# Kernel tuning notes

Measured on AMD Instinct MI355X. Metric: run time of the kernel, lower is better.

The kernel has to match this reference:

```python
import jax, jax.numpy as jnp
import numpy as np

EMBED = 768
HEADS = 12
HEAD_DIM = EMBED // HEADS

def setup_inputs() -> dict:
    key = jax.random.key(0)
    k1, k2, k3, k4 = jax.random.split(key, 4)
    x = jax.random.normal(k1, (8, 1024, EMBED), dtype=jnp.float32)
    # qkv Linear (no bias per qkv_bias=False); proj Linear with bias
    w_qkv = jax.random.normal(k2, (EMBED, 3 * EMBED), dtype=jnp.float32) * 0.02
    w_proj = jax.random.normal(k3, (EMBED, EMBED), dtype=jnp.float32) * 0.02
    b_proj = jax.random.normal(k4, (EMBED,), dtype=jnp.float32) * 0.02
    return {"x": x, "w_qkv": w_qkv, "w_proj": w_proj, "b_proj": b_proj}

def reference(x, w_qkv, w_proj, b_proj):
    b, n, e = x.shape
    h, d = HEADS, HEAD_DIM
    scale = d ** (-0.5)
    qkv = x @ w_qkv                                    # [b, n, 3*e]
    qkv = qkv.reshape(b, n, 3, h, d)                   # (qkv h d) split order
    q, k, v = (jnp.transpose(qkv[:, :, i], (0, 2, 1, 3)) for i in range(3))  # [b,h,n,d]
    dots = jnp.einsum('bhid,bhjd->bhij', q, k) * scale
    attn = jax.nn.softmax(dots, axis=-1)               # dropout p=0 -> identity
    out = jnp.einsum('bhij,bhjd->bhid', attn, v)       # [b,h,n,d]
    out = jnp.transpose(out, (0, 2, 1, 3)).reshape(b, n, e)
    return out @ w_proj + b_proj
```

## Files before the change

### kernel.cpp

```cpp
#include <hip/hip_runtime.h>

typedef _Float16 f16;
typedef _Float16 half8 __attribute__((ext_vector_type(8)));
typedef _Float16 half4v __attribute__((ext_vector_type(4)));
typedef float f32x4 __attribute__((ext_vector_type(4)));

#define MFMA16(a,b,c) __builtin_amdgcn_mfma_f32_16x16x32_f16((a),(b),(c),0,0,0)

__device__ __forceinline__ void gload_lds16(const f16* g, f16* l) {
    __builtin_amdgcn_global_load_lds(
        (const __attribute__((address_space(1))) unsigned int*)g,
        (__attribute__((address_space(3))) unsigned int*)l, 16, 0, 0);
}

__global__ void cast_f32_to_f16(const float* __restrict__ in, f16* __restrict__ out, int n4) {
    int i = blockIdx.x * blockDim.x + threadIdx.x;
    if (i < n4) {
        float4 v = ((const float4*)in)[i];
        half4v h;
        h.x = (f16)v.x; h.y = (f16)v.y; h.z = (f16)v.z; h.w = (f16)v.w;
        ((half4v*)out)[i] = h;
    }
}

__global__ void transpose_cast(const float* __restrict__ in, f16* __restrict__ out, int K, int N) {
    __shared__ f16 tile[32][33];
    int n0 = blockIdx.x * 32, k0 = blockIdx.y * 32;
    int tx = threadIdx.x & 31, ty = threadIdx.x >> 5;
    for (int r = ty; r < 32; r += 8)
        tile[r][tx] = (f16)in[(size_t)(k0 + r) * N + (n0 + tx)];
    __syncthreads();
    for (int r = ty; r < 32; r += 8)
        out[(size_t)(n0 + r) * K + (k0 + tx)] = tile[tx][r];
}

template<int MODE>
__global__ __launch_bounds__(256, 3)
void gemm_bt(const f16* __restrict__ A, const f16* __restrict__ Bt,
             f16* __restrict__ qbuf, f16* __restrict__ kbuf, f16* __restrict__ vtbuf,
             float* __restrict__ out, const float* __restrict__ bias)
{
    constexpr int K = 768;
    constexpr int NX = (MODE == 0) ? 18 : 6;
    constexpr int NWG = NX * 64;
    __shared__ __align__(16) char smem[49152];
    f16* As = (f16*)smem;
    f16* Bs = (f16*)(smem + 24576);
    const int tid  = threadIdx.x;
    const int lane = tid & 63, wave = tid >> 6;
    const int wm = wave >> 1, wn = wave & 1;
    const int l15 = lane & 15, l4 = lane >> 4;

    const int bid = blockIdx.x;
    const int swz = (bid & 7) * (NWG / 8) + (bid >> 3);
    const int m0 = (swz / NX) * 128, n0 = (swz % NX) * 128;

    const int srow  = lane >> 2;
    const int sslot = lane & 3;

    f32x4 acc[4][4] = {};

    #define GSTAGE(buf, kt) do {                                                     \
        _Pragma("unroll")                                                            \
        for (int i = 0; i < 2; ++i) {                                                \
            int rbase = i * 64 + wave * 16;                                          \
            int row = rbase + srow;                                                  \
            gload_lds16(A  + (size_t)(m0 + row) * K + (kt) + sslot * 8, &As[(buf) * 4096 + rbase * 32]); \
            gload_lds16(Bt + (size_t)(n0 + row) * K + (kt) + sslot * 8, &Bs[(buf) * 4096 + rbase * 32]); \
        }                                                                            \
    } while (0)

    GSTAGE(0, 0);
    GSTAGE(1, 32);

    int cur = 0;
    for (int t = 0; t < 24; ++t) {
        if (t < 23) asm volatile("s_waitcnt vmcnt(4)" ::: "memory");
        else        asm volatile("s_waitcnt vmcnt(0)" ::: "memory");
        __builtin_amdgcn_s_barrier();
        if (t < 22) {
            int nb = cur + 2; if (nb >= 3) nb -= 3;
            GSTAGE(nb, (t + 2) * 32);
        }
        half8 af[4], bf[4];
        #pragma unroll
        for (int mi = 0; mi < 4; mi++) af[mi] = *(const half8*)&As[cur*4096 + (wm*64 + mi*16 + l15) * 32 + l4*8];
        #pragma unroll
        for (int ni = 0; ni < 4; ni++) bf[ni] = *(const half8*)&Bs[cur*4096 + (wn*64 + ni*16 + l15) * 32 + l4*8];
        #pragma unroll
        for (int mi = 0; mi < 4; mi++)
            #pragma unroll
            for (int ni = 0; ni < 4; ni++)
                acc[mi][ni] = MFMA16(af[mi], bf[ni], acc[mi][ni]);
        if (++cur >= 3) cur = 0;
    }
    #undef GSTAGE

    if (MODE == 0) {
        __syncthreads();
        f16* sC = (f16*)smem;
        const int t3 = n0 / 768;
        const int bb = m0 >> 10;
        const int mo = m0 & 1023;
        const int h0 = (n0 - t3 * 768) >> 6;

        if (t3 < 2) {
            #pragma unroll
            for (int mi = 0; mi < 4; mi++)
                #pragma unroll
                for (int ni = 0; ni < 4; ni++)
                    #pragma unroll
                    for (int r = 0; r < 4; r++) {
                        int row = wm*64 + mi*16 + l4*4 + r;
                        int col = wn*64 + ni*16 + l15;
                        sC[row * 136 + col] = (f16)acc[mi][ni][r];
                    }
            __syncthreads();
            f16* outb = (t3 == 0) ? qbuf : kbuf;
            #pragma unroll
            for (int hc = 0; hc < 2; hc++) {
                f16* base = outb + ((size_t)(bb * 12 + h0 + hc) * 1024 + mo) * 64;
                #pragma unroll
                for (int i = 0; i < 4; i++) {
                    int row = wave * 32 + i * 8 + (lane >> 3);
                    int cc  = (lane & 7) * 8;
                    half8 v = *(const half8*)&sC[row * 136 + hc * 64 + cc];
                    *(half8*)(base + row * 64 + cc) = v;
                }
            }
        } else {
            #pragma unroll
            for (int mi = 0; mi < 4; mi++)
                #pragma unroll
                for (int ni = 0; ni < 4; ni++) {
                    int row0 = wm*64 + mi*16 + l4*4;
                    int col  = wn*64 + ni*16 + l15;
                    half4v pk;
                    #pragma unroll
                    for (int r = 0; r < 4; r++) pk[r] = (f16)acc[mi][ni][r];
                    *(half4v*)&sC[col * 136 + row0] = pk;
                }
            __syncthreads();
            #pragma unroll
            for (int i = 0; i < 8; i++) {
                int col = wave * 32 + i * 4 + (lane >> 4);
                int rc  = (lane & 15) * 8;
                half8 v = *(const half8*)&sC[col * 136 + rc];
                int head = h0 + (col >> 6), dd = col & 63;
                *(half8*)(vtbuf + ((size_t)(bb * 12 + head) * 64 + dd) * 1024 + mo + rc) = v;
            }
        }
    } else {
        #pragma unroll
        for (int mi = 0; mi < 4; mi++)
            #pragma unroll
            for (int ni = 0; ni < 4; ni++)
                #pragma unroll
                for (int r = 0; r < 4; r++) {
                    int gm = m0 + wm*64 + mi*16 + l4*4 + r;
                    int gn = n0 + wn*64 + ni*16 + l15;
                    out[(size_t)gm * 768 + gn] = acc[mi][ni][r] + bias[gn];
                }
    }
}

__global__ __launch_bounds__(256, 4)
void attn_kernel(const f16* __restrict__ qbuf, const f16* __restrict__ kbuf,
                 const f16* __restrict__ vtbuf, f16* __restrict__ obuf)
{
    __shared__ __align__(16) f16 Ks[2][4096];
    __shared__ __align__(16) f16 Vs[2][4096];
    __shared__ __align__(16) char sPall[4 * 2048];
    const int tid = threadIdx.x;
    const int lane = tid & 63, wave = tid >> 6;
    char* sP = sPall + wave * 2048;
    const int bh = blockIdx.y;
    const int b = bh / 12, h = bh % 12;
    const int q0 = blockIdx.x * 64 + wave * 16;
    const int l15 = lane & 15, l4 = lane >> 4;

    const f16* Q  = qbuf  + (size_t)bh * 65536;
    const f16* Kp = kbuf  + (size_t)bh * 65536;
    const f16* Vt = vtbuf + (size_t)bh * 65536;

    const f16 slh = (f16)(0.125f * 1.44269504089f);
    half8 aq[2];
    aq[0] = *(const half8*)&Q[(q0 + l15) * 64 + l4 * 8];
    aq[1] = *(const half8*)&Q[(q0 + l15) * 64 + 32 + l4 * 8];
    #pragma unroll
    for (int j = 0; j < 8; j++) { aq[0][j] *= slh; aq[1][j] *= slh; }

    const int srow8 = lane >> 3;
    const int c16   = (lane & 7) ^ srow8;

    f32x4 o[4] = {};
    float mrq = -1e30f, lrq = 0.f;

    #define STAGE(buf, kv) do {                                                     \
        _Pragma("unroll")                                                           \
        for (int i = 0; i < 2; ++i) {                                               \
            int rbase = wave * 16 + i * 8;                                          \
            int rl = rbase + srow8;                                                 \
            gload_lds16(Kp + (size_t)((kv) + rl) * 64 + c16 * 8, &Ks[buf][rbase * 64]); \
            gload_lds16(Vt + (size_t)rl * 1024 + (kv) + c16 * 8, &Vs[buf][rbase * 64]); \
        }                                                                           \
    } while (0)

    STAGE(0, 0);
    __syncthreads();

    for (int t = 0; t < 16; ++t) {
        const int cur = t & 1;
        if (t < 15) STAGE(cur ^ 1, (t + 1) * 64);

        const char* Kb = (const char*)&Ks[cur][0];
        const char* Vb = (const char*)&Vs[cur][0];

        f32x4 st[4];
        #pragma unroll
        for (int ni = 0; ni < 4; ni++) {
            int row = ni * 16 + l15;
            int sw = ((row & 7) << 4);
            half8 k0 = *(const half8*)(Kb + row * 128 + ((l4 * 16) ^ sw));
            half8 k1 = *(const half8*)(Kb + row * 128 + ((64 + l4 * 16) ^ sw));
            f32x4 z = {0.f, 0.f, 0.f, 0.f};
            z = MFMA16(k0, aq[0], z);
            st[ni] = MFMA16(k1, aq[1], z);
        }

        float m16 = st[0][0];
        #pragma unroll
        for (int ni = 0; ni < 4; ni++)
            #pragma unroll
            for (int r = 0; r < 4; r++) m16 = fmaxf(m16, st[ni][r]);
        m16 = fmaxf(m16, __shfl_xor(m16, 16));
        m16 = fmaxf(m16, __shfl_xor(m16, 32));

        if (!__all(m16 - mrq <= 11.0f)) {
            float mnew = fmaxf(mrq, m16);
            float alpha = exp2f(mrq - mnew);
            mrq = mnew;
            lrq *= alpha;
            float alr[4];
            #pragma unroll
            for (int r = 0; r < 4; r++) alr[r] = __shfl(alpha, l4*4 + r);
            #pragma unroll
            for (int nd = 0; nd < 4; nd++)
                #pragma unroll
                for (int r = 0; r < 4; r++) o[nd][r] *= alr[r];
        }

        float rs = 0.f;
        #pragma unroll
        for (int ni = 0; ni < 4; ni++)
            #pragma unroll
            for (int r = 0; r < 4; r++) {
                float p = exp2f(st[ni][r] - mrq);
                st[ni][r] = p;
                rs += p;
            }
        rs += __shfl_xor(rs, 16);
        rs += __shfl_xor(rs, 32);
        lrq += rs;

        #pragma unroll
        for (int ni = 0; ni < 4; ni++) {
            half4v pk;
            #pragma unroll
            for (int r = 0; r < 4; r++) pk[r] = (f16)st[ni][r];
            int byte = (l15 * 128 + (ni*16 + l4*4) * 2) ^ ((l15 & 7) << 4);
            *(half4v*)(sP + byte) = pk;
        }

        #pragma unroll
        for (int kk = 0; kk < 2; kk++) {
            int pbyte = (l15 * 128 + (kk*32 + l4*8) * 2) ^ ((l15 & 7) << 4);
            half8 pa = *(const half8*)(sP + pbyte);
            #pragma unroll
            for (int nd = 0; nd < 4; nd++) {
                int row = nd * 16 + l15;
                half8 bv = *(const half8*)(Vb + row * 128 + ((kk*64 + l4*16) ^ ((row & 7) << 4)));
                o[nd] = MFMA16(pa, bv, o[nd]);
            }
        }

        __syncthreads();
    }
    #undef STAGE

    float lrr[4];
    #pragma unroll
    for (int r = 0; r < 4; r++) lrr[r] = 1.f / __shfl(lrq, l4*4 + r);

    f16* Op = obuf + (size_t)b * 1024 * 768 + h * 64;
    #pragma unroll
    for (int nd = 0; nd < 4; nd++)
        #pragma unroll
        for (int r = 0; r < 4; r++) {
            int qi = q0 + l4 * 4 + r;
            int d  = nd * 16 + l15;
            Op[(size_t)qi * 768 + d] = (f16)(o[nd][r] * lrr[r]);
        }
}

extern "C" void kernel_launch(void* const* d_in, const int* in_sizes, int n_in,
                              void* d_out, int out_size, void* d_ws, size_t ws_size,
                              hipStream_t stream) {
    const float* x      = (const float*)d_in[0];
    const float* w_qkv  = (const float*)d_in[1];
    const float* w_proj = (const float*)d_in[2];
    const float* b_proj = (const float*)d_in[3];
    float* out = (float*)d_out;
    char* ws = (char*)d_ws;

    f16* x_h      = (f16*)(ws + 0);
    f16* w_qkv_t  = (f16*)(ws + 12582912);
    f16* w_proj_t = (f16*)(ws + 16121856);
    f16* qb       = (f16*)(ws + 17301504);
    f16* kb       = (f16*)(ws + 29884416);
    f16* vtb      = (f16*)(ws + 42467328);
    f16* ob       = (f16*)(ws + 55050240);

    cast_f32_to_f16<<<dim3(6144), dim3(256), 0, stream>>>(x, x_h, 6291456 / 4);
    transpose_cast<<<dim3(2304 / 32, 768 / 32), dim3(256), 0, stream>>>(w_qkv, w_qkv_t, 768, 2304);
    transpose_cast<<<dim3(768 / 32, 768 / 32), dim3(256), 0, stream>>>(w_proj, w_proj_t, 768, 768);
    gemm_bt<0><<<dim3(18 * 64), dim3(256), 0, stream>>>(
        x_h, w_qkv_t, qb, kb, vtb, nullptr, nullptr);
    attn_kernel<<<dim3(1024 / 64, 96), dim3(256), 0, stream>>>(qb, kb, vtb, ob);
    gemm_bt<1><<<dim3(6 * 64), dim3(256), 0, stream>>>(
        ob, w_proj_t, nullptr, nullptr, nullptr, out, b_proj);
}
```

Before: 137.7 us.

## Fold max subtraction into MFMA init and compute row sums via MFMA

The running max is now folded into the QK^T MFMA accumulator init, so scores arrive already shifted and no per-element subtraction is needed. The softmax row sum is computed by an extra MFMA of the fp16 P tile against a ones vector instead of scalar adds plus cross-lane shuffles. Exponentials are packed with cvt_pkrtz. The row sum now comes from the rounded fp16 probabilities and uses round-toward-zero conversion, which slightly changes numerics. The initial max of 0 relies on the lazy-rescale threshold.

Result: no change. 135.8 us (-1.4%).

```diff
diff --git a/kernel.cpp b/kernel.cpp
--- a/kernel.cpp
+++ b/kernel.cpp
@@ -3,6 +3,7 @@
 typedef _Float16 f16;
 typedef _Float16 half8 __attribute__((ext_vector_type(8)));
 typedef _Float16 half4v __attribute__((ext_vector_type(4)));
+typedef __fp16 fp16x2 __attribute__((ext_vector_type(2)));
 typedef float f32x4 __attribute__((ext_vector_type(4)));
 
 #define MFMA16(a,b,c) __builtin_amdgcn_mfma_f32_16x16x32_f16((a),(b),(c),0,0,0)
@@ -190,11 +191,16 @@
     #pragma unroll
     for (int j = 0; j < 8; j++) { aq[0][j] *= slh; aq[1][j] *= slh; }
 
+    half8 ones;
+    #pragma unroll
+    for (int j = 0; j < 8; j++) ones[j] = (f16)1.0f;
+
     const int srow8 = lane >> 3;
     const int c16   = (lane & 7) ^ srow8;
 
     f32x4 o[4] = {};
-    float mrq = -1e30f, lrq = 0.f;
+    float lr4[4] = {0.f, 0.f, 0.f, 0.f};
+    float mrq = 0.f;
 
     #define STAGE(buf, kv) do {                                                     \
         _Pragma("unroll")                                                           \
@@ -217,61 +223,57 @@
         const char* Vb = (const char*)&Vs[cur][0];
 
         f32x4 st[4];
+        f32x4 zinit = {-mrq, -mrq, -mrq, -mrq};
         #pragma unroll
         for (int ni = 0; ni < 4; ni++) {
             int row = ni * 16 + l15;
             int sw = ((row & 7) << 4);
             half8 k0 = *(const half8*)(Kb + row * 128 + ((l4 * 16) ^ sw));
             half8 k1 = *(const half8*)(Kb + row * 128 + ((64 + l4 * 16) ^ sw));
-            f32x4 z = {0.f, 0.f, 0.f, 0.f};
-            z = MFMA16(k0, aq[0], z);
+            f32x4 z = MFMA16(k0, aq[0], zinit);
             st[ni] = MFMA16(k1, aq[1], z);
         }
 
-        float m16 = st[0][0];
-        #pragma unroll
-        for (int ni = 0; ni < 4; ni++)
-            #pragma unroll
-            for (int r = 0; r < 4; r++) m16 = fmaxf(m16, st[ni][r]);
+        float m16 = fmaxf(fmaxf(st[0][0], st[0][1]), fmaxf(st[0][2], st[0][3]));
+        #pragma unroll
+        for (int ni = 1; ni < 4; ni++) {
+            float a = fmaxf(fmaxf(st[ni][0], st[ni][1]), fmaxf(st[ni][2], st[ni][3]));
+            m16 = fmaxf(m16, a);
+        }
         m16 = fmaxf(m16, __shfl_xor(m16, 16));
         m16 = fmaxf(m16, __shfl_xor(m16, 32));
 
-        if (!__all(m16 - mrq <= 11.0f)) {
-            float mnew = fmaxf(mrq, m16);
-            float alpha = exp2f(mrq - mnew);
-            mrq = mnew;
-            lrq *= alpha;
+        if (!__all(m16 <= 11.0f)) {
+            float d = fmaxf(m16, 0.f);
+            float alpha = exp2f(-d);
+            mrq += d;
+            #pragma unroll
+            for (int ni = 0; ni < 4; ni++)
+                #pragma unroll
+                for (int r = 0; r < 4; r++) st[ni][r] -= d;
             float alr[4];
             #pragma unroll
             for (int r = 0; r < 4; r++) alr[r] = __shfl(alpha, l4*4 + r);
             #pragma unroll
+            for (int r = 0; r < 4; r++) lr4[r] *= alr[r];
+            #pragma unroll
             for (int nd = 0; nd < 4; nd++)
                 #pragma unroll
                 for (int r = 0; r < 4; r++) o[nd][r] *= alr[r];
         }
 
-        float rs = 0.f;
-        #pragma unroll
-        for (int ni = 0; ni < 4; ni++)
-            #pragma unroll
-            for (int r = 0; r < 4; r++) {
-                float p = exp2f(st[ni][r] - mrq);
-                st[ni][r] = p;
-                rs += p;
-            }
-        rs += __shfl_xor(rs, 16);
-        rs += __shfl_xor(rs, 32);
-        lrq += rs;
-
         #pragma unroll
         for (int ni = 0; ni < 4; ni++) {
-            half4v pk;
-            #pragma unroll
-            for (int r = 0; r < 4; r++) pk[r] = (f16)st[ni][r];
+            fp16x2 lo = __builtin_amdgcn_cvt_pkrtz(exp2f(st[ni][0]), exp2f(st[ni][1]));
+            fp16x2 hi = __builtin_amdgcn_cvt_pkrtz(exp2f(st[ni][2]), exp2f(st[ni][3]));
+            uint2 u;
+            u.x = __builtin_bit_cast(unsigned int, lo);
+            u.y = __builtin_bit_cast(unsigned int, hi);
             int byte = (l15 * 128 + (ni*16 + l4*4) * 2) ^ ((l15 & 7) << 4);
-            *(half4v*)(sP + byte) = pk;
-        }
-
+            *(uint2*)(sP + byte) = u;
+        }
+
+        f32x4 racc = {0.f, 0.f, 0.f, 0.f};
         #pragma unroll
         for (int kk = 0; kk < 2; kk++) {
             int pbyte = (l15 * 128 + (kk*32 + l4*8) * 2) ^ ((l15 & 7) << 4);
@@ -282,7 +284,10 @@
                 half8 bv = *(const half8*)(Vb + row * 128 + ((kk*64 + l4*16) ^ ((row & 7) << 4)));
                 o[nd] = MFMA16(pa, bv, o[nd]);
             }
-        }
+            racc = MFMA16(pa, ones, racc);
+        }
+        #pragma unroll
+        for (int r = 0; r < 4; r++) lr4[r] += racc[r];
 
         __syncthreads();
     }
@@ -290,7 +295,7 @@
 
     float lrr[4];
     #pragma unroll
-    for (int r = 0; r < 4; r++) lrr[r] = 1.f / __shfl(lrq, l4*4 + r);
+    for (int r = 0; r < 4; r++) lrr[r] = 1.f / lr4[r];
 
     f16* Op = obuf + (size_t)b * 1024 * 768 + h * 64;
     #pragma unroll
```

## Switch attention kernel to 32x32 MFMA tiles with 128-query blocks

Applied to the files above, without the earlier changes.

Rewrites the attention kernel around the 32x32x16 MFMA so each wave handles 32 query rows and each block 128 queries. Each K/V tile staged in LDS is therefore reused by twice as many queries, and fewer instructions are spent on the score and PV products. The running max is folded into the accumulator initial value, exponentials are packed with cvt_pkrtz, and the grid is reordered so blocks for the same head launch together. In exchange the kernel uses more registers and LDS, the launch bound drops from 4 to 3 blocks, and the grid shrinks to 768 blocks, which may reduce occupancy.

After: 127.6 us. 1.08x faster.

```diff
diff --git a/kernel.cpp b/kernel.cpp
--- a/kernel.cpp
+++ b/kernel.cpp
@@ -3,9 +3,12 @@
 typedef _Float16 f16;
 typedef _Float16 half8 __attribute__((ext_vector_type(8)));
 typedef _Float16 half4v __attribute__((ext_vector_type(4)));
+typedef __fp16 fp16x2 __attribute__((ext_vector_type(2)));
 typedef float f32x4 __attribute__((ext_vector_type(4)));
+typedef float f32x16 __attribute__((ext_vector_type(16)));
 
 #define MFMA16(a,b,c) __builtin_amdgcn_mfma_f32_16x16x32_f16((a),(b),(c),0,0,0)
+#define MFMA32(a,b,c) __builtin_amdgcn_mfma_f32_32x32x16_f16((a),(b),(c),0,0,0)
 
 __device__ __forceinline__ void gload_lds16(const f16* g, f16* l) {
     __builtin_amdgcn_global_load_lds(
@@ -164,37 +167,40 @@
     }
 }
 
-__global__ __launch_bounds__(256, 4)
+__global__ __launch_bounds__(256, 3)
 void attn_kernel(const f16* __restrict__ qbuf, const f16* __restrict__ kbuf,
                  const f16* __restrict__ vtbuf, f16* __restrict__ obuf)
 {
     __shared__ __align__(16) f16 Ks[2][4096];
     __shared__ __align__(16) f16 Vs[2][4096];
-    __shared__ __align__(16) char sPall[4 * 2048];
+    __shared__ __align__(16) char sPall[4 * 4096];
     const int tid = threadIdx.x;
     const int lane = tid & 63, wave = tid >> 6;
-    char* sP = sPall + wave * 2048;
-    const int bh = blockIdx.y;
+    char* sP = sPall + wave * 4096;
+    const int bh = blockIdx.x;
     const int b = bh / 12, h = bh % 12;
-    const int q0 = blockIdx.x * 64 + wave * 16;
-    const int l15 = lane & 15, l4 = lane >> 4;
+    const int q0 = blockIdx.y * 128 + wave * 32;
+    const int l31 = lane & 31, hi = lane >> 5;
+    const int sw0 = (l31 & 7) << 4;
 
     const f16* Q  = qbuf  + (size_t)bh * 65536;
     const f16* Kp = kbuf  + (size_t)bh * 65536;
     const f16* Vt = vtbuf + (size_t)bh * 65536;
 
     const f16 slh = (f16)(0.125f * 1.44269504089f);
-    half8 aq[2];
-    aq[0] = *(const half8*)&Q[(q0 + l15) * 64 + l4 * 8];
-    aq[1] = *(const half8*)&Q[(q0 + l15) * 64 + 32 + l4 * 8];
+    half8 aq[4];
     #pragma unroll
-    for (int j = 0; j < 8; j++) { aq[0][j] *= slh; aq[1][j] *= slh; }
+    for (int c = 0; c < 4; c++) {
+        aq[c] = *(const half8*)&Q[(size_t)(q0 + l31) * 64 + c * 16 + hi * 8];
+        #pragma unroll
+        for (int j = 0; j < 8; j++) aq[c][j] *= slh;
+    }
 
     const int srow8 = lane >> 3;
     const int c16   = (lane & 7) ^ srow8;
 
-    f32x4 o[4] = {};
-    float mrq = -1e30f, lrq = 0.f;
+    f32x16 o0 = {}, o1 = {};
+    float lrq = 0.f, mrq = 0.f;
 
     #define STAGE(buf, kv) do {                                                     \
         _Pragma("unroll")                                                           \
@@ -216,91 +222,83 @@
         const char* Kb = (const char*)&Ks[cur][0];
         const char* Vb = (const char*)&Vs[cur][0];
 
-        f32x4 st[4];
-        #pragma unroll
-        for (int ni = 0; ni < 4; ni++) {
-            int row = ni * 16 + l15;
-            int sw = ((row & 7) << 4);
-            half8 k0 = *(const half8*)(Kb + row * 128 + ((l4 * 16) ^ sw));
-            half8 k1 = *(const half8*)(Kb + row * 128 + ((64 + l4 * 16) ^ sw));
-            f32x4 z = {0.f, 0.f, 0.f, 0.f};
-            z = MFMA16(k0, aq[0], z);
-            st[ni] = MFMA16(k1, aq[1], z);
-        }
-
-        float m16 = st[0][0];
-        #pragma unroll
-        for (int ni = 0; ni < 4; ni++)
-            #pragma unroll
-            for (int r = 0; r < 4; r++) m16 = fmaxf(m16, st[ni][r]);
-        m16 = fmaxf(m16, __shfl_xor(m16, 16));
+        f32x16 st0, st1;
+        #pragma unroll
+        for (int j = 0; j < 16; j++) { st0[j] = -mrq; st1[j] = -mrq; }
+        #pragma unroll
+        for (int c = 0; c < 4; c++) {
+            int koff = (c * 32 + hi * 16) ^ sw0;
+            half8 k0 = *(const half8*)(Kb + l31 * 128 + koff);
+            half8 k1 = *(const half8*)(Kb + (32 + l31) * 128 + koff);
+            st0 = MFMA32(k0, aq[c], st0);
+            st1 = MFMA32(k1, aq[c], st1);
+        }
+
+        float m16 = st0[0];
+        #pragma unroll
+        for (int j = 1; j < 16; j++) m16 = fmaxf(m16, st0[j]);
+        #pragma unroll
+        for (int j = 0; j < 16; j++) m16 = fmaxf(m16, st1[j]);
         m16 = fmaxf(m16, __shfl_xor(m16, 32));
 
-        if (!__all(m16 - mrq <= 11.0f)) {
-            float mnew = fmaxf(mrq, m16);
-            float alpha = exp2f(mrq - mnew);
-            mrq = mnew;
+        if (!__all(m16 <= 11.0f)) {
+            float d = fmaxf(m16, 0.f);
+            float alpha = exp2f(-d);
+            mrq += d;
+            #pragma unroll
+            for (int j = 0; j < 16; j++) { st0[j] -= d; st1[j] -= d; }
             lrq *= alpha;
-            float alr[4];
-            #pragma unroll
-            for (int r = 0; r < 4; r++) alr[r] = __shfl(alpha, l4*4 + r);
-            #pragma unroll
-            for (int nd = 0; nd < 4; nd++)
-                #pragma unroll
-                for (int r = 0; r < 4; r++) o[nd][r] *= alr[r];
+            #pragma unroll
+            for (int reg = 0; reg < 16; reg++) {
+                float a = __shfl(alpha, (reg & 3) + 8 * (reg >> 2) + 4 * hi);
+                o0[reg] *= a; o1[reg] *= a;
+            }
         }
 
         float rs = 0.f;
-        #pragma unroll
-        for (int ni = 0; ni < 4; ni++)
-            #pragma unroll
-            for (int r = 0; r < 4; r++) {
-                float p = exp2f(st[ni][r] - mrq);
-                st[ni][r] = p;
-                rs += p;
-            }
-        rs += __shfl_xor(rs, 16);
+        #define PSTORE(stv, tile) do {                                              \
+            _Pragma("unroll")                                                       \
+            for (int g = 0; g < 4; g++) {                                           \
+                float e0 = exp2f(stv[4*g+0]), e1 = exp2f(stv[4*g+1]);               \
+                float e2 = exp2f(stv[4*g+2]), e3 = exp2f(stv[4*g+3]);               \
+                rs += (e0 + e1) + (e2 + e3);                                        \
+                uint2 u;                                                            \
+                u.x = __builtin_bit_cast(unsigned int, __builtin_amdgcn_cvt_pkrtz(e0, e1)); \
+                u.y = __builtin_bit_cast(unsigned int, __builtin_amdgcn_cvt_pkrtz(e2, e3)); \
+                int byte = (l31 * 128 + ((tile) * 32 + g * 8 + hi * 4) * 2) ^ sw0;  \
+                *(uint2*)(sP + byte) = u;                                           \
+            }                                                                       \
+        } while (0)
+        PSTORE(st0, 0);
+        PSTORE(st1, 1);
+        #undef PSTORE
         rs += __shfl_xor(rs, 32);
         lrq += rs;
 
         #pragma unroll
-        for (int ni = 0; ni < 4; ni++) {
-            half4v pk;
-            #pragma unroll
-            for (int r = 0; r < 4; r++) pk[r] = (f16)st[ni][r];
-            int byte = (l15 * 128 + (ni*16 + l4*4) * 2) ^ ((l15 & 7) << 4);
-            *(half4v*)(sP + byte) = pk;
-        }
-
-        #pragma unroll
-        for (int kk = 0; kk < 2; kk++) {
-            int pbyte = (l15 * 128 + (kk*32 + l4*8) * 2) ^ ((l15 & 7) << 4);
-            half8 pa = *(const half8*)(sP + pbyte);
-            #pragma unroll
-            for (int nd = 0; nd < 4; nd++) {
-                int row = nd * 16 + l15;
-                half8 bv = *(const half8*)(Vb + row * 128 + ((kk*64 + l4*16) ^ ((row & 7) << 4)));
-                o[nd] = MFMA16(pa, bv, o[nd]);
-            }
+        for (int kc = 0; kc < 4; kc++) {
+            int koff = (kc * 32 + hi * 16) ^ sw0;
+            half8 pa = *(const half8*)(sP + l31 * 128 + koff);
+            half8 v0 = *(const half8*)(Vb + l31 * 128 + koff);
+            half8 v1 = *(const half8*)(Vb + (32 + l31) * 128 + koff);
+            o0 = MFMA32(pa, v0, o0);
+            o1 = MFMA32(pa, v1, o1);
         }
 
         __syncthreads();
     }
     #undef STAGE
 
-    float lrr[4];
-    #pragma unroll
-    for (int r = 0; r < 4; r++) lrr[r] = 1.f / __shfl(lrq, l4*4 + r);
-
+    float rq = 1.0f / lrq;
     f16* Op = obuf + (size_t)b * 1024 * 768 + h * 64;
     #pragma unroll
-    for (int nd = 0; nd < 4; nd++)
-        #pragma unroll
-        for (int r = 0; r < 4; r++) {
-            int qi = q0 + l4 * 4 + r;
-            int d  = nd * 16 + l15;
-            Op[(size_t)qi * 768 + d] = (f16)(o[nd][r] * lrr[r]);
-        }
+    for (int reg = 0; reg < 16; reg++) {
+        int qrow = (reg & 3) + 8 * (reg >> 2) + 4 * hi;
+        float inv = __shfl(rq, qrow);
+        size_t base = (size_t)(q0 + qrow) * 768;
+        Op[base + l31]      = (f16)(o0[reg] * inv);
+        Op[base + 32 + l31] = (f16)(o1[reg] * inv);
+    }
 }
 
 extern "C" void kernel_launch(void* const* d_in, const int* in_sizes, int n_in,
@@ -326,7 +324,7 @@
     transpose_cast<<<dim3(768 / 32, 768 / 32), dim3(256), 0, stream>>>(w_proj, w_proj_t, 768, 768);
     gemm_bt<0><<<dim3(18 * 64), dim3(256), 0, stream>>>(
         x_h, w_qkv_t, qb, kb, vtb, nullptr, nullptr);
-    attn_kernel<<<dim3(1024 / 64, 96), dim3(256), 0, stream>>>(qb, kb, vtb, ob);
+    attn_kernel<<<dim3(96, 8), dim3(256), 0, stream>>>(qb, kb, vtb, ob);
     gemm_bt<1><<<dim3(6 * 64), dim3(256), 0, stream>>>(
         ob, w_proj_t, nullptr, nullptr, nullptr, out, b_proj);
 }
```
